# Kernel tuning notes

Hardware: AMD Instinct MI355X
Metric: run time of the kernel (lower is better)

The kernel has to match this reference:

```python
import jax, jax.numpy as jnp
import numpy as np

HID, H, KV, D = 2048, 16, 4, 128
ROPE_THETA = 10000.0
GATE_NORM = 16.0


def _rope_cos_sin(n, d, dtype=jnp.float32):
    inv_freq = 1.0 / (ROPE_THETA ** (jnp.arange(0, d, 2, dtype=jnp.float32) / d))
    freqs = jnp.arange(n, dtype=jnp.float32)[:, None] * inv_freq[None, :]  # (n, d/2)
    cos = jnp.cos(freqs).astype(dtype)[None, :, None, :]  # (1, n, 1, d/2)
    sin = jnp.sin(freqs).astype(dtype)[None, :, None, :]
    return cos, sin


def _apply_rotary(x, cos, sin):
    # x: (b, n, h, d); rotate-half (NeoX) convention over full head dim
    x1, x2 = jnp.split(x, 2, axis=-1)
    return jnp.concatenate([x1 * cos - x2 * sin, x2 * cos + x1 * sin], axis=-1)


def setup_inputs() -> dict:
    key = jax.random.key(0)
    k1, k2, k3, k4, k5 = jax.random.split(key, 5)
    s = 0.02  # realistic init scale for weights
    return {
        "hidden_states": jax.random.normal(k1, (1, 2048, HID), dtype=jnp.float32),
        "Wq": jax.random.normal(k2, (HID, H * D), dtype=jnp.float32) * s,
        "Wk": jax.random.normal(k3, (HID, KV * D), dtype=jnp.float32) * s,
        "Wv": jax.random.normal(k4, (HID, KV * D), dtype=jnp.float32) * s,
        "Wo": jax.random.normal(k5, (H * D, HID), dtype=jnp.float32) * s,
    }


def _forward(hidden_states, Wq, Wk, Wv, Wo):
    b, n, _ = hidden_states.shape
    groups = H // KV

    q = hidden_states @ Wq            # (b, n, H*D)
    k = hidden_states @ Wk            # (b, n, KV*D)
    v = hidden_states @ Wv            # (b, n, KV*D)
    # pool_g: AdaptiveAvgPool1d(KV*D) on a length-(KV*D) last dim == identity
    g = k

    q = q.reshape(b, n, H, D)
    k = k.reshape(b, n, KV, D)
    v = v.reshape(b, n, KV, D)
    g = g.reshape(b, n, KV, D)

    # GQA repeat to H heads
    k = jnp.repeat(k, groups, axis=2)
    v = jnp.repeat(v, groups, axis=2)
    g = jnp.repeat(g, groups, axis=2)

    sq, sk, sv = q, k, v  # raw (pre-softmax) tensors for the attention branch

    # GLA branch inputs: softmax'd q/k, log-sigmoid gates
    qs = jax.nn.softmax(q.astype(jnp.float32), axis=-1)
    ks = jax.nn.softmax(k.astype(jnp.float32), axis=-1)
    gl = jax.nn.log_sigmoid(g.astype(jnp.float32)) / GATE_NORM

    # rotary on raw q/k (seqlen_offset = 0)
    cos, sin = _rope_cos_sin(n, D)
    sq = _apply_rotary(sq, cos, sin)
    sk = _apply_rotary(sk, cos, sin)

    # --- gated linear attention recurrence (chunk_gla math, scale=1) ---
    def step(S, inp):
        q_t, k_t, v_t, g_t = inp  # each (b, H, D)
        S = S * jnp.exp(g_t)[..., None] + k_t[..., None] * v_t[..., None, :]
        o_t = jnp.einsum('bhk,bhkv->bhv', q_t, S)
        return S, o_t

    xs = tuple(jnp.moveaxis(a, 1, 0) for a in (qs, ks, v, gl))  # (n, b, H, D)
    S0 = jnp.zeros((b, H, D, D), dtype=jnp.float32)
    _, o_gla = jax.lax.scan(step, S0, xs)
    o_gla = jnp.moveaxis(o_gla, 0, 1)  # (b, n, H, D)

    # --- causal softmax attention (flash_attn_func, full window) ---
    scale = D ** -0.5
    scores = jnp.einsum('bqhd,bkhd->bhqk', sq, sk) * scale
    causal = jnp.tril(jnp.ones((n, n), dtype=bool))
    scores = jnp.where(causal[None, None], scores, jnp.finfo(scores.dtype).min)
    attn = jax.nn.softmax(scores, axis=-1)
    y = jnp.einsum('bhqk,bkhd->bqhd', attn, sv)

    o = 0.5 * y + 0.5 * o_gla
    o = o.reshape(b, n, H * D).astype(hidden_states.dtype)
    return o @ Wo


def reference(hidden_states, Wq, Wk, Wv, Wo):
    return _forward(hidden_states, Wq, Wk, Wv, Wo)
```

## Files before the change

kernel.cpp:

```cpp
#include <hip/hip_runtime.h>
#include <hip/hip_bf16.h>

typedef __bf16 bf16x8 __attribute__((ext_vector_type(8)));
typedef float f32x4 __attribute__((ext_vector_type(4)));
typedef float f32x16 __attribute__((ext_vector_type(16)));
typedef unsigned u32x4 __attribute__((ext_vector_type(4)));

#define MFMA16(a,b,c) __builtin_amdgcn_mfma_f32_16x16x32_bf16((a),(b),(c),0,0,0)
#define MFMA32(a,b,c) __builtin_amdgcn_mfma_f32_32x32x16_bf16((a),(b),(c),0,0,0)

__device__ __forceinline__ float bf2f(const __hip_bfloat16 h){ return __bfloat162float(h); }
__device__ __forceinline__ __hip_bfloat16 f2bf(float f){ return __float2bfloat16(f); }
__device__ __forceinline__ __bf16 f2raw(float f){
  return __builtin_bit_cast(__bf16, __builtin_bit_cast(unsigned short, __float2bfloat16(f)));
}

__device__ __forceinline__ unsigned pk2(float a, float b){
  unsigned lo = __builtin_bit_cast(unsigned short, __float2bfloat16(a));
  unsigned hi = __builtin_bit_cast(unsigned short, __float2bfloat16(b));
  return lo | (hi << 16);
}
__device__ __forceinline__ void pl32swap(unsigned &x, unsigned &y){
  asm volatile("v_permlane32_swap_b32 %0, %1" : "+v"(x), "+v"(y));
}
__device__ __forceinline__ void gload16(const void* g, void* l){
  __builtin_amdgcn_global_load_lds((const __attribute__((address_space(1))) unsigned int*)g,
                                   (__attribute__((address_space(3))) unsigned int*)l, 16, 0, 0);
}

__device__ __forceinline__ size_t pk_idx(int grp, int ntile, int t, int d){
  int t32 = t >> 5, ql = t & 31, i = d >> 4, kh = (d >> 3) & 1, j = d & 7;
  return ((size_t)(grp*ntile + t32)*8 + i)*512 + (kh*32 + ql)*8 + j;
}

__global__ void k_rope_table(float* __restrict__ ct, float* __restrict__ st){
  int e = blockIdx.x*256 + threadIdx.x;
  if (e >= 2048*64) return;
  int t = e >> 6, d = e & 63;
  float inv = expf(-(float)d * 0.14391156831212787f);
  float ang = (float)t * inv;
  ct[e] = cosf(ang);
  st[e] = sinf(ang);
}

__global__ void k_cvt_bf16(const float* __restrict__ in, __hip_bfloat16* __restrict__ out, int n4){
  int i = blockIdx.x*256 + threadIdx.x;
  if (i >= n4) return;
  float4 v = reinterpret_cast<const float4*>(in)[i];
  ushort4 o;
  o.x = __builtin_bit_cast(unsigned short, f2bf(v.x));
  o.y = __builtin_bit_cast(unsigned short, f2bf(v.y));
  o.z = __builtin_bit_cast(unsigned short, f2bf(v.z));
  o.w = __builtin_bit_cast(unsigned short, f2bf(v.w));
  reinterpret_cast<ushort4*>(out)[i] = o;
}

__global__ __launch_bounds__(256) void k_transpose_bf16(const float* __restrict__ in,
                                                        __hip_bfloat16* __restrict__ out,
                                                        int R, int C, int ldIn){
  __shared__ float tile[64][65];
  int ct_ = blockIdx.x*64, rt = blockIdx.y*64;
  int tx = threadIdx.x & 63, ty = threadIdx.x >> 6;
  #pragma unroll
  for (int i=0;i<16;++i){ int lr = i*4 + ty; tile[lr][tx] = in[(size_t)(rt+lr)*ldIn + ct_+tx]; }
  __syncthreads();
  #pragma unroll
  for (int i=0;i<16;++i){ int lr = i*4 + ty; out[(size_t)(ct_+lr)*R + rt+tx] = f2bf(tile[tx][lr]); }
}

__global__ __launch_bounds__(256) void k_gemm_lds(const __hip_bfloat16* __restrict__ A,
                                                  const __hip_bfloat16* __restrict__ BT,
                                                  float* __restrict__ C, int M, int N, int K){
  __shared__ __hip_bfloat16 As[128*64];
  __shared__ __hip_bfloat16 Bs[128*64];
  int bm = blockIdx.y*128, bn = blockIdx.x*128;
  int tid = threadIdx.x, w = tid >> 6, l = tid & 63, lr = l & 15, lg = l >> 4;
  int wr = (w >> 1)*64, wc = (w & 1)*64;
  int srow = w*32 + (l >> 3);
  int scol = (l & 7)*8;
  const __hip_bfloat16* ga = &A[(size_t)(bm+srow)*K + scol];
  const __hip_bfloat16* gb = &BT[(size_t)(bn+srow)*K + scol];
  __hip_bfloat16* la = &As[w*2048];
  __hip_bfloat16* lb = &Bs[w*2048];
  f32x4 z = {0.f,0.f,0.f,0.f};
  f32x4 acc[4][4];
  #pragma unroll
  for (int i=0;i<4;++i){
    #pragma unroll
    for (int j=0;j<4;++j) acc[i][j] = z;
  }
  for (int bk=0; bk<K; bk+=64){
    #pragma unroll
    for (int i=0;i<4;++i){
      gload16(ga + (size_t)i*8*K + bk, la + i*512);
      gload16(gb + (size_t)i*8*K + bk, lb + i*512);
    }
    __syncthreads();
    __builtin_amdgcn_s_setprio(1);
    #pragma unroll
    for (int kk=0; kk<2; ++kk){
      bf16x8 af[4], bfr[4];
      #pragma unroll
      for (int mi=0;mi<4;++mi) af[mi]  = *reinterpret_cast<const bf16x8*>(&As[(wr+mi*16+lr)*64 + kk*32 + lg*8]);
      #pragma unroll
      for (int ni=0;ni<4;++ni) bfr[ni] = *reinterpret_cast<const bf16x8*>(&Bs[(wc+ni*16+lr)*64 + kk*32 + lg*8]);
      #pragma unroll
      for (int mi=0;mi<4;++mi){
        #pragma unroll
        for (int ni=0;ni<4;++ni)
          acc[mi][ni] = MFMA16(af[mi], bfr[ni], acc[mi][ni]);
      }
    }
    __builtin_amdgcn_s_setprio(0);
    __syncthreads();
  }
  #pragma unroll
  for (int mi=0;mi<4;++mi){
    #pragma unroll
    for (int ni=0;ni<4;++ni){
      #pragma unroll
      for (int r=0;r<4;++r)
        C[(size_t)(bm+wr+mi*16+lg*4+r)*N + (bn+wc+ni*16+lr)] = acc[mi][ni][r];
    }
  }
}

__global__ __launch_bounds__(256) void k_qpost(const float* __restrict__ qkv, const float* __restrict__ ct,
                                              const float* __restrict__ st,
                                              __hip_bfloat16* __restrict__ qs, __hip_bfloat16* __restrict__ qpk){
  int g = blockIdx.x*4 + (threadIdx.x >> 6);
  int t = g >> 4, h = g & 15, i = threadIdx.x & 63;
  size_t base = (size_t)t*3072 + h*128;
  float a = qkv[base + i], b = qkv[base + 64 + i];
  float mx = fmaxf(a,b);
  #pragma unroll
  for (int off=1; off<64; off<<=1) mx = fmaxf(mx, __shfl_xor(mx, off));
  float ea = expf(a-mx), eb = expf(b-mx);
  float sm = ea+eb;
  #pragma unroll
  for (int off=1; off<64; off<<=1) sm += __shfl_xor(sm, off);
  float r = 1.0f/sm;
  size_t ob = ((size_t)t*16 + h)*128;
  qs[ob+i]    = f2bf(ea*r);
  qs[ob+64+i] = f2bf(eb*r);
  const float scale = 0.12751745f;
  float co = ct[t*64+i], si = st[t*64+i];
  qpk[pk_idx(h, 64, t, i)]    = f2bf((a*co - b*si)*scale);
  qpk[pk_idx(h, 64, t, 64+i)] = f2bf((b*co + a*si)*scale);
}

__global__ __launch_bounds__(256) void k_kpost(const float* __restrict__ qkv, const float* __restrict__ ct,
                                              const float* __restrict__ st,
                                              __hip_bfloat16* __restrict__ ks, __hip_bfloat16* __restrict__ kpk){
  int g = blockIdx.x*4 + (threadIdx.x >> 6);
  int t = g >> 2, kv = g & 3, i = threadIdx.x & 63;
  size_t base = (size_t)t*3072 + 2048 + kv*128;
  float a = qkv[base + i], b = qkv[base + 64 + i];
  float mx = fmaxf(a,b);
  #pragma unroll
  for (int off=1; off<64; off<<=1) mx = fmaxf(mx, __shfl_xor(mx, off));
  float ea = expf(a-mx), eb = expf(b-mx);
  float sm = ea+eb;
  #pragma unroll
  for (int off=1; off<64; off<<=1) sm += __shfl_xor(sm, off);
  float r = 1.0f/sm;
  size_t ob = ((size_t)t*4 + kv)*128;
  ks[ob+i]    = f2bf(ea*r);
  ks[ob+64+i] = f2bf(eb*r);
  float co = ct[t*64+i], si = st[t*64+i];
  kpk[pk_idx(kv, 64, t, i)]    = f2bf(a*co - b*si);
  kpk[pk_idx(kv, 64, t, 64+i)] = f2bf(b*co + a*si);
}

__global__ __launch_bounds__(256) void k_vpack(const __hip_bfloat16* __restrict__ vt,
                                               __hip_bfloat16* __restrict__ vpk,
                                               __hip_bfloat16* __restrict__ vpk16){
  int s = blockIdx.x, kv = blockIdx.y;
  int tid = threadIdx.x, l = tid & 63;
  int dt = tid >> 6;
  #pragma unroll
  for (int kq=0; kq<4; ++kq){
    bf16x8 v = *reinterpret_cast<const bf16x8*>(&vt[((size_t)kv*128 + dt*32 + (l&31))*2048 + s*64 + kq*16 + (l>>5)*8]);
    *reinterpret_cast<bf16x8*>(&vpk[((((size_t)kv*32 + s)*4 + dt)*4 + kq)*512 + l*8]) = v;
  }
  #pragma unroll
  for (int idx=0; idx<4; ++idx){
    int oc = dt*2 + (idx>>1), f2 = idx&1;
    bf16x8 v = *reinterpret_cast<const bf16x8*>(&vt[((size_t)kv*128 + oc*16 + (l&15))*2048 + s*64 + f2*32 + (l>>4)*8]);
    *reinterpret_cast<bf16x8*>(&vpk16[((((size_t)kv*32 + s)*8 + oc)*2 + f2)*512 + l*8]) = v;
  }
}

__global__ __launch_bounds__(128) void k_gates(const float* __restrict__ qkv,
                                               float* __restrict__ bt_all,
                                               float* __restrict__ eC){
  int c = blockIdx.x, kv = blockIdx.y, k = threadIdx.x;
  float b = 0.f;
  #pragma unroll 8
  for (int t=0;t<64;++t){
    float x = qkv[(size_t)(c*64+t)*3072 + 2048 + kv*128 + k];
    float gl = (fminf(x,0.f) - log1pf(expf(-fabsf(x)))) * 0.09016844005f;
    b += gl;
    bt_all[(size_t)(c*64+t)*512 + kv*128 + k] = b;
  }
  eC[((size_t)kv*32 + c)*128 + k] = exp2f(b);
}

__global__ __launch_bounds__(256) void k_qeke(const float* __restrict__ bt_all,
                                              const __hip_bfloat16* __restrict__ qs,
                                              const __hip_bfloat16* __restrict__ ks,
                                              __hip_bfloat16* __restrict__ qep,
                                              __hip_bfloat16* __restrict__ ke,
                                              __hip_bfloat16* __restrict__ kep){
  int id = blockIdx.x, tid = threadIdx.x;
  if (id < 2048){
    int t = id, h = tid >> 4, k0 = (tid & 15)*8;
    const float* bp = &bt_all[(size_t)t*512 + (h>>2)*128 + k0];
    bf16x8 q = *reinterpret_cast<const bf16x8*>(&qs[((size_t)t*16 + h)*128 + k0]);
    bf16x8 o;
    #pragma unroll
    for (int j=0;j<8;++j) o[j] = f2raw(exp2f(bp[j]) * (float)q[j]);
    int t16 = t >> 4, lr = t & 15, f = k0 >> 5, lg = (k0 >> 3) & 3;
    *reinterpret_cast<bf16x8*>(&qep[(((size_t)h*128 + t16)*4 + f)*512 + (lg*16+lr)*8]) = o;
  } else {
    int b4 = id - 2048;
    int t = b4*4 + (tid >> 6), kv = (tid >> 4) & 3, k0 = (tid & 15)*8;
    const float* bp = &bt_all[(size_t)t*512 + kv*128 + k0];
    bf16x8 s = *reinterpret_cast<const bf16x8*>(&ks[((size_t)t*4 + kv)*128 + k0]);
    bf16x8 o;
    #pragma unroll
    for (int j=0;j<8;++j) o[j] = f2raw(exp2f(-bp[j]) * (float)s[j]);
    *reinterpret_cast<bf16x8*>(&ke[((size_t)t*4 + kv)*128 + k0]) = o;
    int t16 = t >> 4, lr = t & 15, f = k0 >> 5, lg = (k0 >> 3) & 3;
    *reinterpret_cast<bf16x8*>(&kep[(((size_t)kv*128 + t16)*4 + f)*512 + (lg*16+lr)*8]) = o;
  }
}

__global__ __launch_bounds__(256) void k_ckv(const __hip_bfloat16* __restrict__ ke,
                                             const __hip_bfloat16* __restrict__ vt,
                                             float* __restrict__ ckv){
  __shared__ __hip_bfloat16 kt[128*72];
  int c = blockIdx.x, kv = blockIdx.y;
  int tid = threadIdx.x, w = tid>>6, l = tid&63, lr=l&15, lg=l>>4;
  int wr = (w>>1)*64, wc = (w&1)*64;
  #pragma unroll
  for (int r=0;r<4;++r){
    int idx = r*256 + tid;
    int t  = idx >> 4;
    int k0 = (idx & 15)*8;
    bf16x8 v = *reinterpret_cast<const bf16x8*>(&ke[((size_t)(c*64+t)*4 + kv)*128 + k0]);
    #pragma unroll
    for (int j=0;j<8;++j) kt[(k0+j)*72 + t] = __builtin_bit_cast(__hip_bfloat16, (unsigned short)__builtin_bit_cast(unsigned short, v[j]));
  }
  __syncthreads();
  f32x4 z = {0.f,0.f,0.f,0.f};
  f32x4 acc[4][4];
  #pragma unroll
  for (int i=0;i<4;++i){
    #pragma unroll
    for (int j=0;j<4;++j) acc[i][j]=z;
  }
  size_t sb = (size_t)kv*32 + c;
  #pragma unroll
  for (int kf2=0;kf2<2;++kf2){
    bf16x8 af[4], bfr[4];
    #pragma unroll
    for (int mi=0;mi<4;++mi)
      af[mi] = *reinterpret_cast<const bf16x8*>(&kt[(wr+mi*16+lr)*72 + kf2*32 + lg*8]);
    #pragma unroll
    for (int ni=0;ni<4;++ni)
      bfr[ni] = *reinterpret_cast<const bf16x8*>(&vt[((size_t)kv*128 + wc+ni*16+lr)*2048 + c*64 + kf2*32 + lg*8]);
    #pragma unroll
    for (int mi=0;mi<4;++mi){
      #pragma unroll
      for (int ni=0;ni<4;++ni)
        acc[mi][ni] = MFMA16(af[mi], bfr[ni], acc[mi][ni]);
    }
  }
  #pragma unroll
  for (int mi=0;mi<4;++mi){
    #pragma unroll
    for (int ni=0;ni<4;++ni){
      #pragma unroll
      for (int r=0;r<4;++r)
        ckv[(sb*128 + wr+mi*16+lg*4+r)*128 + wc+ni*16+lr] = acc[mi][ni][r];
    }
  }
}

__global__ __launch_bounds__(256) void k_scan(const float* __restrict__ ckv, const float* __restrict__ eC,
                                              __hip_bfloat16* __restrict__ Stp){
  __shared__ float lds[8*128];
  int kv = blockIdx.y, bx = blockIdx.x;
  int tid = threadIdx.x;
  int eid = tid*4;
  int kloc = eid >> 7;
  int kd  = bx*8 + kloc;
  int vd  = eid & 127;
  int oc = tid >> 5, lr = (tid >> 1) & 15, jh = (tid & 1)*4;
  int f  = bx >> 2, lg = bx & 3;
  float s0=0.f,s1=0.f,s2=0.f,s3=0.f;
  for (int c=0;c<32;++c){
    size_t sb = (size_t)kv*32 + c;
    float4 cur = {s0,s1,s2,s3};
    *reinterpret_cast<float4*>(&lds[kloc*128 + vd]) = cur;
    __syncthreads();
    unsigned w0 = pk2(lds[(jh+0)*128 + oc*16+lr], lds[(jh+1)*128 + oc*16+lr]);
    unsigned w1 = pk2(lds[(jh+2)*128 + oc*16+lr], lds[(jh+3)*128 + oc*16+lr]);
    unsigned* dst = reinterpret_cast<unsigned*>(&Stp[((sb*8+oc)*4+f)*512 + (lg*16+lr)*8 + jh]);
    dst[0]=w0; dst[1]=w1;
    __syncthreads();
    float e = eC[sb*128 + kd];
    float4 u = reinterpret_cast<const float4*>(&ckv[(sb*128 + kd)*128 + vd])[0];
    s0 = (s0 + u.x)*e; s1 = (s1 + u.y)*e; s2 = (s2 + u.z)*e; s3 = (s3 + u.w)*e;
  }
}

__global__ __launch_bounds__(256) void k_attn(const __hip_bfloat16* __restrict__ qpk,
                                              const __hip_bfloat16* __restrict__ kpk,
                                              const __hip_bfloat16* __restrict__ vpk,
                                              float* __restrict__ ocomb){
  __shared__ __hip_bfloat16 OW[4][32][138];
  __shared__ float mW[4][32], lW[4][32];
  int h = blockIdx.y, kvh = h >> 2;
  int tid = threadIdx.x, w = tid >> 6, l = tid & 63;
  int ql = l & 31, kh = l >> 5;

  #pragma unroll 1
  for (int half=0; half<2; ++half){
    int qt = half ? (63 - (int)blockIdx.x) : (int)blockIdx.x;
    int qbase = qt*32;
    int qg = qbase + ql;

    bf16x8 qf[8];
    #pragma unroll
    for (int i=0;i<8;++i)
      qf[i] = *reinterpret_cast<const bf16x8*>(&qpk[((size_t)(h*64 + qt)*8 + i)*512 + l*8]);

    f32x16 zz = {0.f,0.f,0.f,0.f,0.f,0.f,0.f,0.f,0.f,0.f,0.f,0.f,0.f,0.f,0.f,0.f};
    f32x16 of[4];
    #pragma unroll
    for (int dt=0;dt<4;++dt) of[dt] = zz;
    float m = -1e30f, ll = 0.f;

    int nstep = qt/2 + 1;
    for (int s=w; s<nstep; s+=4){
      int kb = s*64;
      bool last = (s == nstep-1);
      f32x16 s0 = zz, s1 = zz;
      #pragma unroll
      for (int i=0;i<8;++i){
        bf16x8 k0 = *reinterpret_cast<const bf16x8*>(&kpk[((size_t)(kvh*64 + 2*s)*8 + i)*512 + l*8]);
        s0 = MFMA32(k0, qf[i], s0);
      }
      #pragma unroll
      for (int i=0;i<8;++i){
        bf16x8 k1 = *reinterpret_cast<const bf16x8*>(&kpk[((size_t)(kvh*64 + 2*s+1)*8 + i)*512 + l*8]);
        s1 = MFMA32(k1, qf[i], s1);
      }
      if (last){
        #pragma unroll
        for (int r=0;r<16;++r){
          int kr = (r&3) + 8*(r>>2) + 4*kh;
          if (kb + kr > qg)      s0[r] = -1e30f;
          if (kb + 32 + kr > qg) s1[r] = -1e30f;
        }
      }
      float pmax = fmaxf(s0[0], s1[0]);
      #pragma unroll
      for (int r=1;r<16;++r) pmax = fmaxf(pmax, fmaxf(s0[r], s1[r]));
      pmax = fmaxf(pmax, __shfl_xor(pmax, 32));
      if (!__all(pmax <= m + 11.54f)){
        float nm = fmaxf(m, pmax);
        float ef = exp2f(m - nm);
        ll *= ef;
        #pragma unroll
        for (int dt=0;dt<4;++dt){
          #pragma unroll
          for (int r=0;r<16;++r) of[dt][r] *= ef;
        }
        m = nm;
      }
      float ps = 0.f;
      #pragma unroll
      for (int r=0;r<16;++r){ s0[r] = exp2f(s0[r]-m); ps += s0[r]; }
      #pragma unroll
      for (int r=0;r<16;++r){ s1[r] = exp2f(s1[r]-m); ps += s1[r]; }
      ps += __shfl_xor(ps, 32);
      ll += ps;
      unsigned pw[4][4];
      {
        unsigned a,b;
        a = pk2(s0[0],s0[1]);   b = pk2(s0[4],s0[5]);   pl32swap(a,b); pw[0][0]=a; pw[0][2]=b;
        a = pk2(s0[2],s0[3]);   b = pk2(s0[6],s0[7]);   pl32swap(a,b); pw[0][1]=a; pw[0][3]=b;
        a = pk2(s0[8],s0[9]);   b = pk2(s0[12],s0[13]); pl32swap(a,b); pw[1][0]=a; pw[1][2]=b;
        a = pk2(s0[10],s0[11]); b = pk2(s0[14],s0[15]); pl32swap(a,b); pw[1][1]=a; pw[1][3]=b;
        a = pk2(s1[0],s1[1]);   b = pk2(s1[4],s1[5]);   pl32swap(a,b); pw[2][0]=a; pw[2][2]=b;
        a = pk2(s1[2],s1[3]);   b = pk2(s1[6],s1[7]);   pl32swap(a,b); pw[2][1]=a; pw[2][3]=b;
        a = pk2(s1[8],s1[9]);   b = pk2(s1[12],s1[13]); pl32swap(a,b); pw[3][0]=a; pw[3][2]=b;
        a = pk2(s1[10],s1[11]); b = pk2(s1[14],s1[15]); pl32swap(a,b); pw[3][1]=a; pw[3][3]=b;
      }
      #pragma unroll
      for (int dt=0; dt<4; ++dt){
        #pragma unroll
        for (int kq=0; kq<4; ++kq){
          bf16x8 vf = *reinterpret_cast<const bf16x8*>(&vpk[((((size_t)kvh*32 + s)*4 + dt)*4 + kq)*512 + l*8]);
          u32x4 pu = {pw[kq][0], pw[kq][1], pw[kq][2], pw[kq][3]};
          bf16x8 pb = __builtin_bit_cast(bf16x8, pu);
          of[dt] = MFMA32(vf, pb, of[dt]);
        }
      }
    }
    if (kh == 0){ mW[w][ql] = m; lW[w][ql] = ll; }
    #pragma unroll
    for (int dt=0; dt<4; ++dt){
      #pragma unroll
      for (int rp=0; rp<4; ++rp){
        unsigned lo = pk2(of[dt][rp*4+0], of[dt][rp*4+1]);
        unsigned hi = pk2(of[dt][rp*4+2], of[dt][rp*4+3]);
        unsigned* dst = reinterpret_cast<unsigned*>(&OW[w][ql][dt*32 + 8*rp + 4*kh]);
        dst[0] = lo; dst[1] = hi;
      }
    }
    __syncthreads();
    int q = tid >> 3, db = (tid & 7)*16;
    float m0=mW[0][q], m1=mW[1][q], m2=mW[2][q], m3=mW[3][q];
    float ms = fmaxf(fmaxf(m0,m1), fmaxf(m2,m3));
    float fac[4] = {exp2f(m0-ms), exp2f(m1-ms), exp2f(m2-ms), exp2f(m3-ms)};
    float lt = fac[0]*lW[0][q] + fac[1]*lW[1][q] + fac[2]*lW[2][q] + fac[3]*lW[3][q];
    float acc[16];
    #pragma unroll
    for (int j=0;j<16;++j) acc[j] = 0.f;
    #pragma unroll
    for (int wv=0; wv<4; ++wv){
      const unsigned* src = reinterpret_cast<const unsigned*>(&OW[wv][q][db]);
      float fx = fac[wv];
      #pragma unroll
      for (int j=0;j<8;++j){
        unsigned u = src[j];
        acc[2*j]   += fx * __builtin_bit_cast(float, u << 16);
        acc[2*j+1] += fx * __builtin_bit_cast(float, u & 0xffff0000u);
      }
    }
    float inv = 0.5f / lt;
    float4 o0 = {acc[0]*inv, acc[1]*inv, acc[2]*inv, acc[3]*inv};
    float4 o1 = {acc[4]*inv, acc[5]*inv, acc[6]*inv, acc[7]*inv};
    float4 o2 = {acc[8]*inv, acc[9]*inv, acc[10]*inv, acc[11]*inv};
    float4 o3 = {acc[12]*inv, acc[13]*inv, acc[14]*inv, acc[15]*inv};
    float4* dst = reinterpret_cast<float4*>(&ocomb[(size_t)(qbase+q)*2048 + h*128 + db]);
    dst[0]=o0; dst[1]=o1; dst[2]=o2; dst[3]=o3;
    __syncthreads();
  }
}

__global__ __launch_bounds__(256) void k_gla_out(const __hip_bfloat16* __restrict__ qep,
                                                 const __hip_bfloat16* __restrict__ kep,
                                                 const __hip_bfloat16* __restrict__ vpk16,
                                                 const __hip_bfloat16* __restrict__ Stp,
                                                 const float* __restrict__ ocomb,
                                                 __hip_bfloat16* __restrict__ obf){
  __shared__ __hip_bfloat16 ldsp[4*16*72];
  int c = blockIdx.x, h = blockIdx.y, kvh = h >> 2;
  int tid = threadIdx.x, w = tid>>6, l = tid&63, lr = l&15, lg = l>>4;
  int t0 = c*64, r0 = w*16;
  __hip_bfloat16* myp = &ldsp[w*16*72];
  bf16x8 qef[4];
  #pragma unroll
  for (int f=0; f<4; ++f)
    qef[f] = *reinterpret_cast<const bf16x8*>(&qep[(((size_t)h*128 + c*4 + w)*4 + f)*512 + l*8]);
  f32x4 z = {0.f,0.f,0.f,0.f};
  f32x4 of[8];
  #pragma unroll
  for (int oc=0;oc<8;++oc) of[oc]=z;
  __builtin_amdgcn_s_setprio(1);
  #pragma unroll
  for (int oc=0; oc<8; ++oc){
    #pragma unroll
    for (int f=0; f<4; ++f){
      bf16x8 sfr = *reinterpret_cast<const bf16x8*>(&Stp[((((size_t)kvh*32 + c)*8 + oc)*4 + f)*512 + l*8]);
      of[oc] = MFMA16(qef[f], sfr, of[oc]);
    }
  }
  f32x4 sacc[4] = {z,z,z,z};
  #pragma unroll
  for (int cb=0; cb<4; ++cb){
    #pragma unroll
    for (int f=0; f<4; ++f){
      bf16x8 kf = *reinterpret_cast<const bf16x8*>(&kep[(((size_t)kvh*128 + c*4 + cb)*4 + f)*512 + l*8]);
      sacc[cb] = MFMA16(qef[f], kf, sacc[cb]);
    }
  }
  __builtin_amdgcn_s_setprio(0);
  #pragma unroll
  for (int cb=0; cb<4; ++cb){
    #pragma unroll
    for (int r=0;r<4;++r){
      int s_ = cb*16 + lr;
      int t_ = r0 + lg*4 + r;
      float v = (s_ <= t_) ? sacc[cb][r] : 0.f;
      myp[(lg*4 + r)*72 + cb*16 + lr] = f2bf(v);
    }
  }
  bf16x8 pf[2];
  #pragma unroll
  for (int kf2=0;kf2<2;++kf2)
    pf[kf2] = *reinterpret_cast<const bf16x8*>(&myp[lr*72 + kf2*32 + lg*8]);
  __builtin_amdgcn_s_setprio(1);
  #pragma unroll
  for (int oc=0; oc<8; ++oc){
    #pragma unroll
    for (int kf2=0;kf2<2;++kf2){
      bf16x8 vf = *reinterpret_cast<const bf16x8*>(&vpk16[((((size_t)kvh*32 + c)*8 + oc)*2 + kf2)*512 + l*8]);
      of[oc] = MFMA16(pf[kf2], vf, of[oc]);
    }
  }
  __builtin_amdgcn_s_setprio(0);
  #pragma unroll
  for (int oc=0;oc<8;++oc){
    #pragma unroll
    for (int r=0;r<4;++r){
      int row = t0 + r0 + lg*4 + r;
      int col = h*128 + oc*16 + lr;
      float prev = ocomb[(size_t)row*2048 + col];
      obf[(size_t)row*2048 + col] = f2bf(prev + 0.5f*of[oc][r]);
    }
  }
}

extern "C" void kernel_launch(void* const* d_in, const int* in_sizes, int n_in,
                              void* d_out, int out_size, void* d_ws, size_t ws_size,
                              hipStream_t stream) {
  const float* hs = (const float*)d_in[0];
  const float* Wq = (const float*)d_in[1];
  const float* Wk = (const float*)d_in[2];
  const float* Wv = (const float*)d_in[3];
  const float* Wo = (const float*)d_in[4];
  float* out = (float*)d_out;

  char* base = (char*)d_ws;
  size_t off = 0;
  auto alloc = [&](size_t bytes) -> void* {
    void* p = base + off;
    off = (off + bytes + 255) & ~(size_t)255;
    return p;
  };

  float*          ropeC  = (float*)alloc(2048*64*4);
  float*          ropeS  = (float*)alloc(2048*64*4);
  __hip_bfloat16* hsb    = (__hip_bfloat16*)alloc((size_t)4194304*2);
  __hip_bfloat16* WqkvT  = (__hip_bfloat16*)alloc((size_t)3072*2048*2);
  __hip_bfloat16* WoT    = (__hip_bfloat16*)alloc((size_t)4194304*2);
  float*          qkv    = (float*)alloc((size_t)2048*3072*4);
  __hip_bfloat16* qpk    = (__hip_bfloat16*)alloc((size_t)4194304*2);
  __hip_bfloat16* ks     = (__hip_bfloat16*)alloc((size_t)1048576*2);
  __hip_bfloat16* kpk    = (__hip_bfloat16*)alloc((size_t)1048576*2);
  __hip_bfloat16* vt     = (__hip_bfloat16*)alloc((size_t)1048576*2);
  __hip_bfloat16* vpk    = (__hip_bfloat16*)alloc((size_t)1048576*2);
  __hip_bfloat16* vpk16  = (__hip_bfloat16*)alloc((size_t)1048576*2);
  __hip_bfloat16* qep    = (__hip_bfloat16*)alloc((size_t)4194304*2);
  __hip_bfloat16* ke     = (__hip_bfloat16*)alloc((size_t)1048576*2);
  __hip_bfloat16* kep    = (__hip_bfloat16*)alloc((size_t)1048576*2);
  float*          bt_all = (float*)alloc((size_t)1048576*4);
  float*          eC     = (float*)alloc((size_t)4*32*128*4);
  float*          ckv    = (float*)alloc((size_t)4*32*128*128*4);
  __hip_bfloat16* Stp    = (__hip_bfloat16*)alloc((size_t)4*32*128*128*2);
  __hip_bfloat16* qs     = (__hip_bfloat16*)ckv;
  float*          ocomb  = qkv;
  __hip_bfloat16* obf    = hsb;

  if (off > ws_size) return;

  k_rope_table<<<512, 256, 0, stream>>>(ropeC, ropeS);
  k_cvt_bf16<<<4096, 256, 0, stream>>>(hs, hsb, 1048576);
  k_transpose_bf16<<<dim3(32,32), 256, 0, stream>>>(Wq, WqkvT, 2048, 2048, 2048);
  k_transpose_bf16<<<dim3(8,32),  256, 0, stream>>>(Wk, WqkvT + (size_t)2048*2048, 2048, 512, 512);
  k_transpose_bf16<<<dim3(8,32),  256, 0, stream>>>(Wv, WqkvT + (size_t)2560*2048, 2048, 512, 512);
  k_transpose_bf16<<<dim3(32,32), 256, 0, stream>>>(Wo, WoT, 2048, 2048, 2048);

  k_gemm_lds<<<dim3(24,16), 256, 0, stream>>>(hsb, WqkvT, qkv, 2048, 3072, 2048);

  k_qpost<<<dim3(8192), 256, 0, stream>>>(qkv, ropeC, ropeS, qs, qpk);
  k_kpost<<<dim3(2048), 256, 0, stream>>>(qkv, ropeC, ropeS, ks, kpk);
  k_transpose_bf16<<<dim3(8,32), 256, 0, stream>>>(qkv + 2560, vt, 2048, 512, 3072);
  k_vpack<<<dim3(32,4), 256, 0, stream>>>(vt, vpk, vpk16);
  k_gates<<<dim3(32,4), 128, 0, stream>>>(qkv, bt_all, eC);

  k_qeke<<<dim3(2560), 256, 0, stream>>>(bt_all, qs, ks, qep, ke, kep);
  k_ckv<<<dim3(32,4), 256, 0, stream>>>(ke, vt, ckv);
  k_scan<<<dim3(16,4), 256, 0, stream>>>(ckv, eC, Stp);

  k_attn<<<dim3(32,16), 256, 0, stream>>>(qpk, kpk, vpk, ocomb);
  k_gla_out<<<dim3(32,16), 256, 0, stream>>>(qep, kep, vpk16, Stp, ocomb, obf);

  k_gemm_lds<<<dim3(16,16), 256, 0, stream>>>(obf, WoT, out, 2048, 2048, 2048);
}
```

Measured before the change: 296.6 us.

## Merge weight transposes, retile GEMMs to 128x64 with XCD swizzle, prefetch scan loads

Merges the four weight transpose launches into a single kernel. Replaces the 128x128, 4-wave GEMM with a 128x64, 2-wave tile, which doubles the number of workgroups. Workgroup IDs are remapped so that neighbouring tiles land on the same XCD, for better L2 reuse. The chunk scan now prefetches the next chunk's gate and ckv values to hide load latency. Smaller tiles mean more operand reloads per FLOP.

Measured after the change: 279.5 us. 1.06x faster.

```diff
diff --git a/kernel.cpp b/kernel.cpp
--- a/kernel.cpp
+++ b/kernel.cpp
@@ -68,20 +68,44 @@
   for (int i=0;i<16;++i){ int lr = i*4 + ty; out[(size_t)(ct_+lr)*R + rt+tx] = f2bf(tile[tx][lr]); }
 }
 
-__global__ __launch_bounds__(256) void k_gemm_lds(const __hip_bfloat16* __restrict__ A,
-                                                  const __hip_bfloat16* __restrict__ BT,
-                                                  float* __restrict__ C, int M, int N, int K){
+__global__ __launch_bounds__(256) void k_transpose_w(const float* __restrict__ Wq,
+                                                     const float* __restrict__ Wk,
+                                                     const float* __restrict__ Wv,
+                                                     const float* __restrict__ Wo,
+                                                     __hip_bfloat16* __restrict__ WqkvT,
+                                                     __hip_bfloat16* __restrict__ WoT){
+  __shared__ float tile[64][65];
+  int id = blockIdx.x;
+  const float* in; __hip_bfloat16* out; int C, bx, by;
+  if (id < 1024)      { in=Wq; out=WqkvT;                         C=2048; bx=id&31;          by=id>>5; }
+  else if (id < 1280) { int i=id-1024; in=Wk; out=WqkvT+(size_t)2048*2048; C=512; bx=i&7;    by=i>>3; }
+  else if (id < 1536) { int i=id-1280; in=Wv; out=WqkvT+(size_t)2560*2048; C=512; bx=i&7;    by=i>>3; }
+  else                { int i=id-1536; in=Wo; out=WoT;            C=2048; bx=i&31;           by=i>>5; }
+  const int R = 2048;
+  int ct_ = bx*64, rt = by*64;
+  int tx = threadIdx.x & 63, ty = threadIdx.x >> 6;
+  #pragma unroll
+  for (int i=0;i<16;++i){ int lr = i*4 + ty; tile[lr][tx] = in[(size_t)(rt+lr)*C + ct_+tx]; }
+  __syncthreads();
+  #pragma unroll
+  for (int i=0;i<16;++i){ int lr = i*4 + ty; out[(size_t)(ct_+lr)*R + rt+tx] = f2bf(tile[tx][lr]); }
+}
+
+__global__ __launch_bounds__(128) void k_gemm_lds2(const __hip_bfloat16* __restrict__ A,
+                                                   const __hip_bfloat16* __restrict__ BT,
+                                                   float* __restrict__ C, int M, int N, int K){
   __shared__ __hip_bfloat16 As[128*64];
-  __shared__ __hip_bfloat16 Bs[128*64];
-  int bm = blockIdx.y*128, bn = blockIdx.x*128;
+  __shared__ __hip_bfloat16 Bs[64*64];
+  int nwg = gridDim.x;
+  int cpx = nwg >> 3;
+  int wg  = blockIdx.x;
+  int swz = (wg & 7)*cpx + (wg >> 3);
+  int nbx = N >> 6;
+  int bn = (swz % nbx)*64, bm = (swz / nbx)*128;
   int tid = threadIdx.x, w = tid >> 6, l = tid & 63, lr = l & 15, lg = l >> 4;
-  int wr = (w >> 1)*64, wc = (w & 1)*64;
-  int srow = w*32 + (l >> 3);
-  int scol = (l & 7)*8;
-  const __hip_bfloat16* ga = &A[(size_t)(bm+srow)*K + scol];
-  const __hip_bfloat16* gb = &BT[(size_t)(bn+srow)*K + scol];
-  __hip_bfloat16* la = &As[w*2048];
-  __hip_bfloat16* lb = &Bs[w*2048];
+  int wr = w*64;
+  int srow = tid >> 3;
+  int scol = (tid & 7)*8;
   f32x4 z = {0.f,0.f,0.f,0.f};
   f32x4 acc[4][4];
   #pragma unroll
@@ -91,10 +115,11 @@
   }
   for (int bk=0; bk<K; bk+=64){
     #pragma unroll
-    for (int i=0;i<4;++i){
-      gload16(ga + (size_t)i*8*K + bk, la + i*512);
-      gload16(gb + (size_t)i*8*K + bk, lb + i*512);
-    }
+    for (int i=0;i<8;++i)
+      gload16(&A[(size_t)(bm + i*16 + srow)*K + bk + scol], &As[i*1024 + tid*8]);
+    #pragma unroll
+    for (int i=0;i<4;++i)
+      gload16(&BT[(size_t)(bn + i*16 + srow)*K + bk + scol], &Bs[i*1024 + tid*8]);
     __syncthreads();
     __builtin_amdgcn_s_setprio(1);
     #pragma unroll
@@ -103,7 +128,7 @@
       #pragma unroll
       for (int mi=0;mi<4;++mi) af[mi]  = *reinterpret_cast<const bf16x8*>(&As[(wr+mi*16+lr)*64 + kk*32 + lg*8]);
       #pragma unroll
-      for (int ni=0;ni<4;++ni) bfr[ni] = *reinterpret_cast<const bf16x8*>(&Bs[(wc+ni*16+lr)*64 + kk*32 + lg*8]);
+      for (int ni=0;ni<4;++ni) bfr[ni] = *reinterpret_cast<const bf16x8*>(&Bs[(ni*16+lr)*64 + kk*32 + lg*8]);
       #pragma unroll
       for (int mi=0;mi<4;++mi){
         #pragma unroll
@@ -120,7 +145,7 @@
     for (int ni=0;ni<4;++ni){
       #pragma unroll
       for (int r=0;r<4;++r)
-        C[(size_t)(bm+wr+mi*16+lg*4+r)*N + (bn+wc+ni*16+lr)] = acc[mi][ni][r];
+        C[(size_t)(bm+wr+mi*16+lg*4+r)*N + (bn+ni*16+lr)] = acc[mi][ni][r];
     }
   }
 }
@@ -293,15 +318,22 @@
   __shared__ float lds[8*128];
   int kv = blockIdx.y, bx = blockIdx.x;
   int tid = threadIdx.x;
-  int eid = tid*4;
-  int kloc = eid >> 7;
+  int kloc = tid >> 5;
   int kd  = bx*8 + kloc;
-  int vd  = eid & 127;
+  int vd  = (tid*4) & 127;
   int oc = tid >> 5, lr = (tid >> 1) & 15, jh = (tid & 1)*4;
   int f  = bx >> 2, lg = bx & 3;
   float s0=0.f,s1=0.f,s2=0.f,s3=0.f;
+  size_t sb0 = (size_t)kv*32;
+  float e = eC[sb0*128 + kd];
+  float4 u = reinterpret_cast<const float4*>(&ckv[(sb0*128 + kd)*128 + vd])[0];
   for (int c=0;c<32;++c){
-    size_t sb = (size_t)kv*32 + c;
+    size_t sb = sb0 + c;
+    float e_n = 0.f; float4 u_n = {0.f,0.f,0.f,0.f};
+    if (c < 31){
+      e_n = eC[(sb+1)*128 + kd];
+      u_n = reinterpret_cast<const float4*>(&ckv[((sb+1)*128 + kd)*128 + vd])[0];
+    }
     float4 cur = {s0,s1,s2,s3};
     *reinterpret_cast<float4*>(&lds[kloc*128 + vd]) = cur;
     __syncthreads();
@@ -310,9 +342,8 @@
     unsigned* dst = reinterpret_cast<unsigned*>(&Stp[((sb*8+oc)*4+f)*512 + (lg*16+lr)*8 + jh]);
     dst[0]=w0; dst[1]=w1;
     __syncthreads();
-    float e = eC[sb*128 + kd];
-    float4 u = reinterpret_cast<const float4*>(&ckv[(sb*128 + kd)*128 + vd])[0];
     s0 = (s0 + u.x)*e; s1 = (s1 + u.y)*e; s2 = (s2 + u.z)*e; s3 = (s3 + u.w)*e;
+    e = e_n; u = u_n;
   }
 }
 
@@ -572,12 +603,9 @@
 
   k_rope_table<<<512, 256, 0, stream>>>(ropeC, ropeS);
   k_cvt_bf16<<<4096, 256, 0, stream>>>(hs, hsb, 1048576);
-  k_transpose_bf16<<<dim3(32,32), 256, 0, stream>>>(Wq, WqkvT, 2048, 2048, 2048);
-  k_transpose_bf16<<<dim3(8,32),  256, 0, stream>>>(Wk, WqkvT + (size_t)2048*2048, 2048, 512, 512);
-  k_transpose_bf16<<<dim3(8,32),  256, 0, stream>>>(Wv, WqkvT + (size_t)2560*2048, 2048, 512, 512);
-  k_transpose_bf16<<<dim3(32,32), 256, 0, stream>>>(Wo, WoT, 2048, 2048, 2048);
-
-  k_gemm_lds<<<dim3(24,16), 256, 0, stream>>>(hsb, WqkvT, qkv, 2048, 3072, 2048);
+  k_transpose_w<<<dim3(2560), 256, 0, stream>>>(Wq, Wk, Wv, Wo, WqkvT, WoT);
+
+  k_gemm_lds2<<<dim3(768), 128, 0, stream>>>(hsb, WqkvT, qkv, 2048, 3072, 2048);
 
   k_qpost<<<dim3(8192), 256, 0, stream>>>(qkv, ropeC, ropeS, qs, qpk);
   k_kpost<<<dim3(2048), 256, 0, stream>>>(qkv, ropeC, ropeS, ks, kpk);
@@ -592,5 +620,5 @@
   k_attn<<<dim3(32,16), 256, 0, stream>>>(qpk, kpk, vpk, ocomb);
   k_gla_out<<<dim3(32,16), 256, 0, stream>>>(qep, kep, vpk16, Stp, ocomb, obf);
 
-  k_gemm_lds<<<dim3(16,16), 256, 0, stream>>>(obf, WoT, out, 2048, 2048, 2048);
-}
+  k_gemm_lds2<<<dim3(512), 128, 0, stream>>>(obf, WoT, out, 2048, 2048, 2048);
+}
```
